# Kernel optimization log

Measured on AMD Instinct MI355X. Metric: run time of the kernel, lower is better.

Reference implementation:

```python
import jax, jax.numpy as jnp
import numpy as np

N_NODES = 100000
N_EDGES = 3200000
D_FEAT = 64
H_SIZE = 32
N_CLASSES = 10


def setup_inputs() -> dict:
    key = jax.random.key(0)
    ks = jax.random.split(key, 9)
    x = jax.random.normal(ks[0], (N_NODES, D_FEAT), dtype=jnp.float32)
    edge_index = jax.random.randint(ks[1], (2, N_EDGES), 0, N_NODES, dtype=jnp.int64)
    y = jax.random.randint(ks[2], (N_NODES,), 0, N_CLASSES, dtype=jnp.int64)
    s1 = 1.0 / np.sqrt(D_FEAT)
    s2 = 1.0 / np.sqrt(H_SIZE)
    W1_rel = jax.random.uniform(ks[3], (H_SIZE, D_FEAT), jnp.float32, -s1, s1)
    b1_rel = jax.random.uniform(ks[4], (H_SIZE,), jnp.float32, -s1, s1)
    W1_root = jax.random.uniform(ks[5], (H_SIZE, D_FEAT), jnp.float32, -s1, s1)
    W2_rel = jax.random.uniform(ks[6], (N_CLASSES, H_SIZE), jnp.float32, -s2, s2)
    b2_rel = jax.random.uniform(ks[7], (N_CLASSES,), jnp.float32, -s2, s2)
    W2_root = jax.random.uniform(ks[8], (N_CLASSES, H_SIZE), jnp.float32, -s2, s2)
    return {"x": x, "edge_index": edge_index, "y": y,
            "W1_rel": W1_rel, "b1_rel": b1_rel, "W1_root": W1_root,
            "W2_rel": W2_rel, "b2_rel": b2_rel, "W2_root": W2_root}


def _graph_conv(x, src, dst, W_rel, b_rel, W_root):
    # PyG GraphConv (aggr='add'): out_i = W_root x_i + b + W_rel * sum_{j: (j->i)} x_j
    agg = jax.ops.segment_sum(x[src], dst, num_segments=N_NODES)  # [N, d_in]
    return agg @ W_rel.T + b_rel + x @ W_root.T


def reference(x, edge_index, y, W1_rel, b1_rel, W1_root, W2_rel, b2_rel, W2_root):
    src, dst = edge_index[0], edge_index[1]
    h = jax.nn.relu(_graph_conv(x, src, dst, W1_rel, b1_rel, W1_root))  # [N, 32]
    logits = _graph_conv(h, src, dst, W2_rel, b2_rel, W2_root)          # [N, 10]
    logp = jax.nn.log_softmax(logits, axis=-1)
    loss = -jnp.mean(jnp.take_along_axis(logp, y[:, None], axis=-1)[:, 0])
    return loss
```

## Files before the change

kernel.cpp:

```cpp
#include <hip/hip_runtime.h>
#include <hip/hip_bf16.h>
#include <hip/hip_fp8.h>

#define D_FEAT 64
#define H_SIZE 32
#define N_CLASSES 10
#define NPB 256
#define MAXB 512
#define NCHUNK 256
#define BT 1024
#define NT 256
#define CSR_CAP 12032

using short8 = __attribute__((ext_vector_type(8))) short;
using f32x4v = __attribute__((ext_vector_type(4))) float;

__device__ inline short f2bf(float f) {
    __hip_bfloat16 h = __float2bfloat16(f);
    return *reinterpret_cast<short*>(&h);
}

#define F8(u, s) ({ __hip_fp8_e4m3 _f; _f.__x = (unsigned char)(((u) >> (s)) & 0xff); (float)_f; })

#define ACC16(p) do { \
    a[0]  += F8((p).x, 0);  a[1]  += F8((p).x, 8);  a[2]  += F8((p).x, 16); a[3]  += F8((p).x, 24); \
    a[4]  += F8((p).y, 0);  a[5]  += F8((p).y, 8);  a[6]  += F8((p).y, 16); a[7]  += F8((p).y, 24); \
    a[8]  += F8((p).z, 0);  a[9]  += F8((p).z, 8);  a[10] += F8((p).z, 16); a[11] += F8((p).z, 24); \
    a[12] += F8((p).w, 0);  a[13] += F8((p).w, 8);  a[14] += F8((p).w, 16); a[15] += F8((p).w, 24); } while (0)

#define ACC8(p) do { \
    a[0] += __uint_as_float((p).x << 16); a[1] += __uint_as_float((p).x & 0xFFFF0000u); \
    a[2] += __uint_as_float((p).y << 16); a[3] += __uint_as_float((p).y & 0xFFFF0000u); \
    a[4] += __uint_as_float((p).z << 16); a[5] += __uint_as_float((p).z & 0xFFFF0000u); \
    a[6] += __uint_as_float((p).w << 16); a[7] += __uint_as_float((p).w & 0xFFFF0000u); } while (0)


__global__ __launch_bounds__(NT) void dense1_mfma(
    const float* __restrict__ x, const float* __restrict__ W1_rel,
    const float* __restrict__ b1, const float* __restrict__ W1_root,
    unsigned* __restrict__ xr8, float* __restrict__ xroot, int n_nodes) {
    __shared__ unsigned short sW[64 * 72];
    __shared__ float sOut[64 * 65];
    __shared__ float sb[H_SIZE];
    int tid = threadIdx.x;
    for (int i = tid; i < 64 * 64; i += NT) {
        int n = i >> 6, k = i & 63;
        float w = (n < 32) ? W1_rel[n * 64 + k] : W1_root[(n - 32) * 64 + k];
        sW[n * 72 + k] = (unsigned short)f2bf(w);
    }
    if (tid < H_SIZE) sb[tid] = b1[tid];
    __syncthreads();

    int lane = tid & 63, wave = tid >> 6;
    int r16 = lane & 15, h = lane >> 4;

    short8 bf[4][2];
#pragma unroll
    for (int t = 0; t < 4; ++t)
#pragma unroll
        for (int s = 0; s < 2; ++s) {
            const unsigned short* p = &sW[(t * 16 + r16) * 72 + s * 32 + h * 8];
            bf[t][s] = *reinterpret_cast<const short8*>(p);
        }

    int nbase = blockIdx.x * 64 + wave * 16;
    int row = nbase + r16;
    int rowc = min(row, n_nodes - 1);

    short8 af[2];
#pragma unroll
    for (int s = 0; s < 2; ++s) {
        const float* px = x + (size_t)rowc * D_FEAT + s * 32 + h * 8;
        float4 lo = *reinterpret_cast<const float4*>(px);
        float4 hi = *reinterpret_cast<const float4*>(px + 4);
        short8 a;
        a[0] = f2bf(lo.x); a[1] = f2bf(lo.y); a[2] = f2bf(lo.z); a[3] = f2bf(lo.w);
        a[4] = f2bf(hi.x); a[5] = f2bf(hi.y); a[6] = f2bf(hi.z); a[7] = f2bf(hi.w);
        af[s] = a;
    }

    f32x4v acc[4] = {{0.f,0.f,0.f,0.f},{0.f,0.f,0.f,0.f},
                     {0.f,0.f,0.f,0.f},{0.f,0.f,0.f,0.f}};
#pragma unroll
    for (int t = 0; t < 4; ++t) {
        acc[t] = __builtin_amdgcn_mfma_f32_16x16x32_bf16(af[0], bf[t][0], acc[t], 0, 0, 0);
        acc[t] = __builtin_amdgcn_mfma_f32_16x16x32_bf16(af[1], bf[t][1], acc[t], 0, 0, 0);
    }
#pragma unroll
    for (int t = 0; t < 4; ++t)
#pragma unroll
        for (int r = 0; r < 4; ++r)
            sOut[(wave * 16 + h * 4 + r) * 65 + t * 16 + r16] = acc[t][r];
    __syncthreads();

    int nl = lane;
    int g = blockIdx.x * 64 + nl;
    if (g < n_nodes) {
        if (wave < 2) {
            unsigned w4[4];
#pragma unroll
            for (int q = 0; q < 4; ++q) {
                unsigned wd = 0;
#pragma unroll
                for (int b = 0; b < 4; ++b) {
                    float v = sOut[nl * 65 + wave * 16 + q * 4 + b];
                    __hip_fp8_e4m3 f8(v);
                    wd |= ((unsigned)f8.__x) << (8 * b);
                }
                w4[q] = wd;
            }
            *reinterpret_cast<uint4*>(&xr8[(size_t)g * 8 + wave * 4]) =
                make_uint4(w4[0], w4[1], w4[2], w4[3]);
        } else {
            int co = (wave - 2) * 16;
#pragma unroll
            for (int q = 0; q < 4; ++q) {
                float4 v;
                v.x = sOut[nl * 65 + 32 + co + q * 4 + 0] + sb[co + q * 4 + 0];
                v.y = sOut[nl * 65 + 32 + co + q * 4 + 1] + sb[co + q * 4 + 1];
                v.z = sOut[nl * 65 + 32 + co + q * 4 + 2] + sb[co + q * 4 + 2];
                v.w = sOut[nl * 65 + 32 + co + q * 4 + 3] + sb[co + q * 4 + 3];
                *reinterpret_cast<float4*>(&xroot[(size_t)g * 32 + co + q * 4]) = v;
            }
        }
    }
}


__global__ __launch_bounds__(BT) void bucket_count(
    const int* __restrict__ dst, int* __restrict__ counts,
    int* __restrict__ totals, int n_edges, int nbuckets, int ept) {
    __shared__ int hist[MAXB];
    for (int i = threadIdx.x; i < nbuckets; i += BT) hist[i] = 0;
    __syncthreads();
    int beg = blockIdx.x * ept;
    int end = min(beg + ept, n_edges);
    for (int e = beg + threadIdx.x; e < end; e += BT)
        atomicAdd(&hist[dst[e] >> 8], 1);
    __syncthreads();
    for (int b = threadIdx.x; b < nbuckets; b += BT) {
        int h = hist[b];
        counts[b * NCHUNK + blockIdx.x] = h;
        if (h) atomicAdd(&totals[b], h);
    }
}

__global__ __launch_bounds__(MAXB) void scan_small(
    const int* __restrict__ totals, int* __restrict__ bbase, int nbuckets) {
    __shared__ int lds[MAXB];
    int tid = threadIdx.x;
    int v = (tid < nbuckets) ? totals[tid] : 0;
    lds[tid] = v;
    __syncthreads();
    for (int off = 1; off < MAXB; off <<= 1) {
        int t = (tid >= off) ? lds[tid - off] : 0;
        __syncthreads();
        lds[tid] += t;
        __syncthreads();
    }
    if (tid < nbuckets) bbase[tid] = lds[tid] - v;
}

__global__ __launch_bounds__(NPB) void scan_within(
    int* __restrict__ counts, const int* __restrict__ bbase) {
    __shared__ int lds[NPB];
    int b = blockIdx.x, tid = threadIdx.x;
    int v = counts[b * NCHUNK + tid];
    lds[tid] = v;
    __syncthreads();
    for (int off = 1; off < NPB; off <<= 1) {
        int t = (tid >= off) ? lds[tid - off] : 0;
        __syncthreads();
        lds[tid] += t;
        __syncthreads();
    }
    counts[b * NCHUNK + tid] = bbase[b] + lds[tid] - v;
}

__global__ __launch_bounds__(BT) void bucket_scatter(
    const int* __restrict__ src, const int* __restrict__ dst,
    const int* __restrict__ base, unsigned* __restrict__ packed,
    int n_edges, int nbuckets, int ept) {
    __shared__ int cur[MAXB];
    for (int b = threadIdx.x; b < nbuckets; b += BT)
        cur[b] = base[b * NCHUNK + blockIdx.x];
    __syncthreads();
    int beg = blockIdx.x * ept;
    int end = min(beg + ept, n_edges);
    for (int e = beg + threadIdx.x; e < end; e += BT) {
        int s = src[e], d = dst[e];
        int slot = atomicAdd(&cur[d >> 8], 1);
        packed[slot] = (unsigned)s | ((unsigned)(d & 255) << 24);
    }
}


__global__ __launch_bounds__(NPB) void csr_build(
    const unsigned* __restrict__ packed, const int* __restrict__ base,
    int* __restrict__ rowptr, int* __restrict__ csr,
    int n_nodes, int nbuckets, int n_edges) {
    __shared__ int cnt[NPB];
    __shared__ int cur[NPB];
    __shared__ unsigned cache[CSR_CAP];
    int b = blockIdx.x, tid = threadIdx.x;
    int pBeg = base[b * NCHUNK];
    int pEnd = (b + 1 < nbuckets) ? base[(b + 1) * NCHUNK] : n_edges;
    int sz = pEnd - pBeg;
    int m = min(sz, CSR_CAP);
    cnt[tid] = 0;
    for (int i = tid; i < m; i += NPB) cache[i] = packed[pBeg + i];
    __syncthreads();
    for (int i = tid; i < sz; i += NPB) {
        unsigned p = (i < m) ? cache[i] : packed[pBeg + i];
        atomicAdd(&cnt[p >> 24], 1);
    }
    __syncthreads();
    int v = cnt[tid];
    cur[tid] = v;
    __syncthreads();
    for (int off = 1; off < NPB; off <<= 1) {
        int t = (tid >= off) ? cur[tid - off] : 0;
        __syncthreads();
        cur[tid] += t;
        __syncthreads();
    }
    int gbase = pBeg + cur[tid] - v;
    int n = (b << 8) + tid;
    if (n < n_nodes) rowptr[n] = gbase;
    if (b == nbuckets - 1 && tid == 0) rowptr[n_nodes] = n_edges;
    cur[tid] = gbase;
    __syncthreads();
    for (int i = tid; i < sz; i += NPB) {
        unsigned p = (i < m) ? cache[i] : packed[pBeg + i];
        int slot = atomicAdd(&cur[p >> 24], 1);
        csr[slot] = (int)(p & 0xFFFFFF);
    }
}


__global__ __launch_bounds__(NT) void gather1_kernel(
    const uint4* __restrict__ xr8v,
    const float* __restrict__ xroot,
    const int* __restrict__ rowptr, const int* __restrict__ csr,
    const float* __restrict__ W2_rel, const float* __restrict__ b2,
    const float* __restrict__ W2_root,
    __hip_bfloat16* __restrict__ h2, float* __restrict__ hroot, int n_nodes) {
    __shared__ float sWrelT[H_SIZE * 17];
    __shared__ float sWrootT[H_SIZE * 17];
    __shared__ float sb[16];
    __shared__ float sh[128][33];
    int tid = threadIdx.x;
    for (int i = tid; i < H_SIZE * 17; i += NT) { sWrelT[i] = 0.f; sWrootT[i] = 0.f; }
    __syncthreads();
    for (int i = tid; i < N_CLASSES * H_SIZE; i += NT) {
        int c = i >> 5, j = i & 31;
        sWrelT[j * 17 + c] = W2_rel[i];
        sWrootT[j * 17 + c] = W2_root[i];
    }
    if (tid < 16) sb[tid] = (tid < N_CLASSES) ? b2[tid] : 0.f;

    int t = blockIdx.x * NT + tid;
    int n = t >> 1, c1 = t & 1;
    float a[16] = {0.f,0.f,0.f,0.f,0.f,0.f,0.f,0.f,
                   0.f,0.f,0.f,0.f,0.f,0.f,0.f,0.f};
    if (n < n_nodes) {
        int beg = rowptr[n], end = rowptr[n + 1];
        int i = beg;
        for (; i + 8 <= end; i += 8) {
            int e0 = csr[i + c1];
            int e1 = csr[i + 2 + c1];
            int e2 = csr[i + 4 + c1];
            int e3 = csr[i + 6 + c1];
            uint4 p0 = xr8v[(size_t)__shfl(e0, 0, 2) * 2 + c1];
            uint4 p1 = xr8v[(size_t)__shfl(e0, 1, 2) * 2 + c1];
            uint4 p2 = xr8v[(size_t)__shfl(e1, 0, 2) * 2 + c1];
            uint4 p3 = xr8v[(size_t)__shfl(e1, 1, 2) * 2 + c1];
            uint4 p4 = xr8v[(size_t)__shfl(e2, 0, 2) * 2 + c1];
            uint4 p5 = xr8v[(size_t)__shfl(e2, 1, 2) * 2 + c1];
            uint4 p6 = xr8v[(size_t)__shfl(e3, 0, 2) * 2 + c1];
            uint4 p7 = xr8v[(size_t)__shfl(e3, 1, 2) * 2 + c1];
            ACC16(p0); ACC16(p1); ACC16(p2); ACC16(p3);
            ACC16(p4); ACC16(p5); ACC16(p6); ACC16(p7);
        }
        if (i + 4 <= end) {
            int e0 = csr[i + c1];
            int e1 = csr[i + 2 + c1];
            uint4 p0 = xr8v[(size_t)__shfl(e0, 0, 2) * 2 + c1];
            uint4 p1 = xr8v[(size_t)__shfl(e0, 1, 2) * 2 + c1];
            uint4 p2 = xr8v[(size_t)__shfl(e1, 0, 2) * 2 + c1];
            uint4 p3 = xr8v[(size_t)__shfl(e1, 1, 2) * 2 + c1];
            ACC16(p0); ACC16(p1); ACC16(p2); ACC16(p3);
            i += 4;
        }
        if (i + 2 <= end) {
            int e0 = csr[i + c1];
            uint4 p0 = xr8v[(size_t)__shfl(e0, 0, 2) * 2 + c1];
            uint4 p1 = xr8v[(size_t)__shfl(e0, 1, 2) * 2 + c1];
            ACC16(p0); ACC16(p1);
            i += 2;
        }
        if (i < end) {
            int e = csr[i];
            uint4 p = xr8v[(size_t)e * 2 + c1];
            ACC16(p);
        }
        const float4* xr4 = reinterpret_cast<const float4*>(
            xroot + (size_t)n * 32 + c1 * 16);
#pragma unroll
        for (int q = 0; q < 4; ++q) {
            float4 v = xr4[q];
            a[q * 4 + 0] = fmaxf(a[q * 4 + 0] + v.x, 0.f);
            a[q * 4 + 1] = fmaxf(a[q * 4 + 1] + v.y, 0.f);
            a[q * 4 + 2] = fmaxf(a[q * 4 + 2] + v.z, 0.f);
            a[q * 4 + 3] = fmaxf(a[q * 4 + 3] + v.w, 0.f);
        }
    }
    int nl = tid >> 1;
#pragma unroll
    for (int j = 0; j < 16; ++j) sh[nl][c1 * 16 + j] = a[j];
    __syncthreads();

#pragma unroll
    for (int pass = 0; pass < 8; ++pass) {
        int idx = pass * NT + tid;
        int nl2 = idx >> 4, c = idx & 15;
        int n2 = blockIdx.x * 128 + nl2;
        if (n2 < n_nodes) {
            float ar = 0.f, ao = 0.f;
#pragma unroll
            for (int j = 0; j < H_SIZE; ++j) {
                float hv = sh[nl2][j];
                ar += hv * sWrelT[j * 17 + c];
                ao += hv * sWrootT[j * 17 + c];
            }
            h2[(size_t)n2 * 16 + c] = __float2bfloat16(ar);
            hroot[(size_t)n2 * 16 + c] = ao + sb[c];
        }
    }
}


__global__ __launch_bounds__(NT) void gather2_loss_kernel(
    const uint4* __restrict__ h2v,
    const float* __restrict__ hroot,
    const int* __restrict__ rowptr, const int* __restrict__ csr,
    const int* __restrict__ y, float* __restrict__ loss,
    int n_nodes, float invN) {
    int t = blockIdx.x * NT + threadIdx.x;
    int n = t >> 1, c1 = t & 1;
    int lane = threadIdx.x & 63;
    bool active = (n < n_nodes);

    float a[8] = {0.f,0.f,0.f,0.f,0.f,0.f,0.f,0.f};
    int yv = 0;
    if (active) {
        int beg = rowptr[n], end = rowptr[n + 1];
        int i = beg;
        for (; i + 8 <= end; i += 8) {
            int e0 = csr[i + c1];
            int e1 = csr[i + 2 + c1];
            int e2 = csr[i + 4 + c1];
            int e3 = csr[i + 6 + c1];
            uint4 p0 = h2v[(size_t)__shfl(e0, 0, 2) * 2 + c1];
            uint4 p1 = h2v[(size_t)__shfl(e0, 1, 2) * 2 + c1];
            uint4 p2 = h2v[(size_t)__shfl(e1, 0, 2) * 2 + c1];
            uint4 p3 = h2v[(size_t)__shfl(e1, 1, 2) * 2 + c1];
            uint4 p4 = h2v[(size_t)__shfl(e2, 0, 2) * 2 + c1];
            uint4 p5 = h2v[(size_t)__shfl(e2, 1, 2) * 2 + c1];
            uint4 p6 = h2v[(size_t)__shfl(e3, 0, 2) * 2 + c1];
            uint4 p7 = h2v[(size_t)__shfl(e3, 1, 2) * 2 + c1];
            ACC8(p0); ACC8(p1); ACC8(p2); ACC8(p3);
            ACC8(p4); ACC8(p5); ACC8(p6); ACC8(p7);
        }
        if (i + 4 <= end) {
            int e0 = csr[i + c1];
            int e1 = csr[i + 2 + c1];
            uint4 p0 = h2v[(size_t)__shfl(e0, 0, 2) * 2 + c1];
            uint4 p1 = h2v[(size_t)__shfl(e0, 1, 2) * 2 + c1];
            uint4 p2 = h2v[(size_t)__shfl(e1, 0, 2) * 2 + c1];
            uint4 p3 = h2v[(size_t)__shfl(e1, 1, 2) * 2 + c1];
            ACC8(p0); ACC8(p1); ACC8(p2); ACC8(p3);
            i += 4;
        }
        if (i + 2 <= end) {
            int e0 = csr[i + c1];
            uint4 p0 = h2v[(size_t)__shfl(e0, 0, 2) * 2 + c1];
            uint4 p1 = h2v[(size_t)__shfl(e0, 1, 2) * 2 + c1];
            ACC8(p0); ACC8(p1);
            i += 2;
        }
        if (i < end) {
            int e = csr[i];
            uint4 p = h2v[(size_t)e * 2 + c1];
            ACC8(p);
        }
        const float4* hr4 = reinterpret_cast<const float4*>(
            hroot + (size_t)n * 16 + c1 * 8);
        float4 h0 = hr4[0], h1 = hr4[1];
        a[0] += h0.x; a[1] += h0.y; a[2] += h0.z; a[3] += h0.w;
        a[4] += h1.x; a[5] += h1.y; a[6] += h1.z; a[7] += h1.w;
        yv = y[n];
    }
    bool full = active && (c1 == 0);
    float m = -INFINITY;
#pragma unroll
    for (int j = 0; j < 8; ++j) {
        bool v = (j < 2) ? active : full;
        m = fmaxf(m, v ? a[j] : -INFINITY);
    }
    m = fmaxf(m, __shfl_xor(m, 1, 64));
    float es = 0.f;
#pragma unroll
    for (int j = 0; j < 8; ++j) {
        bool v = (j < 2) ? active : full;
        es += v ? expf(a[j] - m) : 0.f;
    }
    es += __shfl_xor(es, 1, 64);
    int yl = yv & 7;
    float lyc = 0.f;
#pragma unroll
    for (int j = 0; j < 8; ++j) lyc = (j == yl) ? a[j] : lyc;
    float ly = __shfl(lyc, (lane & ~1) + (yv >> 3), 64);
    float contrib = (active && c1 == 0) ? (m + logf(es) - ly) * invN : 0.f;

#pragma unroll
    for (int o = 32; o > 0; o >>= 1) contrib += __shfl_down(contrib, o, 64);
    __shared__ float part[NT / 64];
    if (lane == 0) part[threadIdx.x >> 6] = contrib;
    __syncthreads();
    if (threadIdx.x == 0) {
        float v = 0.f;
#pragma unroll
        for (int w = 0; w < NT / 64; ++w) v += part[w];
        atomicAdd(loss, v);
    }
}


extern "C" void kernel_launch(void* const* d_in, const int* in_sizes, int n_in,
                              void* d_out, int out_size, void* d_ws, size_t ws_size,
                              hipStream_t stream) {
    const float* x       = (const float*)d_in[0];
    const int*   ei      = (const int*)d_in[1];
    const int*   y       = (const int*)d_in[2];
    const float* W1_rel  = (const float*)d_in[3];
    const float* b1_rel  = (const float*)d_in[4];
    const float* W1_root = (const float*)d_in[5];
    const float* W2_rel  = (const float*)d_in[6];
    const float* b2_rel  = (const float*)d_in[7];
    const float* W2_root = (const float*)d_in[8];
    float* loss = (float*)d_out;

    const int n_nodes = in_sizes[0] / D_FEAT;
    const int n_edges = in_sizes[1] / 2;
    const int* src = ei;
    const int* dst = ei + n_edges;

    const int nbuckets = (n_nodes + NPB - 1) / NPB;
    const int M = nbuckets * NCHUNK;
    const int ept = (n_edges + NCHUNK - 1) / NCHUNK;

    size_t off = 0;
    auto alloc = [&](size_t bytes) {
        void* p = (char*)d_ws + off;
        off = (off + bytes + 255) & ~(size_t)255;
        return p;
    };
    int*            counts = (int*)alloc((size_t)(M + 1) * 4);
    int*            totals = (int*)alloc((size_t)MAXB * 4);
    int*            bbase  = (int*)alloc((size_t)MAXB * 4);
    unsigned*       packed = (unsigned*)alloc((size_t)n_edges * 4);
    int*            rowptr = (int*)alloc((size_t)(n_nodes + 1) * 4);
    int*            csr    = (int*)alloc((size_t)n_edges * 4);
    unsigned*       xr8    = (unsigned*)alloc((size_t)n_nodes * 32);
    float*          xroot  = (float*)alloc((size_t)n_nodes * H_SIZE * 4);
    __hip_bfloat16* h2     = (__hip_bfloat16*)alloc((size_t)n_nodes * 16 * 2);
    float*          hroot  = (float*)alloc((size_t)n_nodes * 16 * 4);

    dense1_mfma<<<(n_nodes + 63) / 64, NT, 0, stream>>>(
        x, W1_rel, b1_rel, W1_root, xr8, xroot, n_nodes);

    hipMemsetAsync(totals, 0, (size_t)MAXB * 4, stream);
    bucket_count<<<NCHUNK, BT, 0, stream>>>(dst, counts, totals,
                                            n_edges, nbuckets, ept);
    scan_small<<<1, MAXB, 0, stream>>>(totals, bbase, nbuckets);
    scan_within<<<nbuckets, NPB, 0, stream>>>(counts, bbase);
    bucket_scatter<<<NCHUNK, BT, 0, stream>>>(src, dst, counts, packed,
                                              n_edges, nbuckets, ept);
    csr_build<<<nbuckets, NPB, 0, stream>>>(packed, counts, rowptr, csr,
                                            n_nodes, nbuckets, n_edges);

    gather1_kernel<<<(n_nodes + 127) / 128, NT, 0, stream>>>(
        (const uint4*)xr8, xroot, rowptr, csr,
        W2_rel, b2_rel, W2_root, h2, hroot, n_nodes);

    hipMemsetAsync(loss, 0, sizeof(float), stream);
    gather2_loss_kernel<<<(n_nodes + 127) / 128, NT, 0, stream>>>(
        (const uint4*)h2, hroot, rowptr, csr, y, loss,
        n_nodes, 1.f / (float)n_nodes);
}
```

Measured before the change: 158.7 us.

## Store layer-2 message features as FP8 and gather whole rows per thread

gather1 now quantises the 16-wide per-node relation projection to FP8 e4m3 and packs four values per word, giving 16-byte rows instead of 32-byte bf16 rows. gather2 changes from two lanes sharing each neighbour row to each lane of a pair loading full 16-byte rows for alternate edges, then combining the pair with xor shuffles. The log-softmax now runs in a single lane over all 10 classes. The aim is to halve the random-gather traffic in the second aggregation, at the cost of FP8 rounding error in the logits and so in the loss.

After: 155.2 us. -2.3%, faster.

```diff
diff --git a/kernel.cpp b/kernel.cpp
--- a/kernel.cpp
+++ b/kernel.cpp
@@ -28,11 +28,10 @@
     a[8]  += F8((p).z, 0);  a[9]  += F8((p).z, 8);  a[10] += F8((p).z, 16); a[11] += F8((p).z, 24); \
     a[12] += F8((p).w, 0);  a[13] += F8((p).w, 8);  a[14] += F8((p).w, 16); a[15] += F8((p).w, 24); } while (0)
 
-#define ACC8(p) do { \
-    a[0] += __uint_as_float((p).x << 16); a[1] += __uint_as_float((p).x & 0xFFFF0000u); \
-    a[2] += __uint_as_float((p).y << 16); a[3] += __uint_as_float((p).y & 0xFFFF0000u); \
-    a[4] += __uint_as_float((p).z << 16); a[5] += __uint_as_float((p).z & 0xFFFF0000u); \
-    a[6] += __uint_as_float((p).w << 16); a[7] += __uint_as_float((p).w & 0xFFFF0000u); } while (0)
+#define ACC10(p) do { \
+    a[0] += F8((p).x, 0);  a[1] += F8((p).x, 8);  a[2] += F8((p).x, 16); a[3] += F8((p).x, 24); \
+    a[4] += F8((p).y, 0);  a[5] += F8((p).y, 8);  a[6] += F8((p).y, 16); a[7] += F8((p).y, 24); \
+    a[8] += F8((p).z, 0);  a[9] += F8((p).z, 8); } while (0)
 
 
 __global__ __launch_bounds__(NT) void dense1_mfma(
@@ -244,7 +243,7 @@
     const int* __restrict__ rowptr, const int* __restrict__ csr,
     const float* __restrict__ W2_rel, const float* __restrict__ b2,
     const float* __restrict__ W2_root,
-    __hip_bfloat16* __restrict__ h2, float* __restrict__ hroot, int n_nodes) {
+    unsigned* __restrict__ h2b, float* __restrict__ hroot, int n_nodes) {
     __shared__ float sWrelT[H_SIZE * 17];
     __shared__ float sWrootT[H_SIZE * 17];
     __shared__ float sb[16];
@@ -325,15 +324,24 @@
         int idx = pass * NT + tid;
         int nl2 = idx >> 4, c = idx & 15;
         int n2 = blockIdx.x * 128 + nl2;
-        if (n2 < n_nodes) {
-            float ar = 0.f, ao = 0.f;
-#pragma unroll
-            for (int j = 0; j < H_SIZE; ++j) {
-                float hv = sh[nl2][j];
-                ar += hv * sWrelT[j * 17 + c];
-                ao += hv * sWrootT[j * 17 + c];
+        bool valid = (n2 < n_nodes);
+        float ar = 0.f, ao = 0.f;
+#pragma unroll
+        for (int j = 0; j < H_SIZE; ++j) {
+            float hv = sh[nl2][j];
+            ar += hv * sWrelT[j * 17 + c];
+            ao += hv * sWrootT[j * 17 + c];
+        }
+        float r1 = __shfl_down(ar, 1, 64);
+        float r2 = __shfl_down(ar, 2, 64);
+        float r3 = __shfl_down(ar, 3, 64);
+        if (valid) {
+            if ((c & 3) == 0) {
+                __hip_fp8_e4m3 f0(ar), f1(r1), f2(r2), f3(r3);
+                unsigned wd = (unsigned)f0.__x | ((unsigned)f1.__x << 8) |
+                              ((unsigned)f2.__x << 16) | ((unsigned)f3.__x << 24);
+                h2b[(size_t)n2 * 4 + (c >> 2)] = wd;
             }
-            h2[(size_t)n2 * 16 + c] = __float2bfloat16(ar);
             hroot[(size_t)n2 * 16 + c] = ao + sb[c];
         }
     }
@@ -341,7 +349,7 @@
 
 
 __global__ __launch_bounds__(NT) void gather2_loss_kernel(
-    const uint4* __restrict__ h2v,
+    const uint4* __restrict__ h2q,
     const float* __restrict__ hroot,
     const int* __restrict__ rowptr, const int* __restrict__ csr,
     const int* __restrict__ y, float* __restrict__ loss,
@@ -351,8 +359,7 @@
     int lane = threadIdx.x & 63;
     bool active = (n < n_nodes);
 
-    float a[8] = {0.f,0.f,0.f,0.f,0.f,0.f,0.f,0.f};
-    int yv = 0;
+    float a[10] = {0.f,0.f,0.f,0.f,0.f,0.f,0.f,0.f,0.f,0.f};
     if (active) {
         int beg = rowptr[n], end = rowptr[n + 1];
         int i = beg;
@@ -361,67 +368,46 @@
             int e1 = csr[i + 2 + c1];
             int e2 = csr[i + 4 + c1];
             int e3 = csr[i + 6 + c1];
-            uint4 p0 = h2v[(size_t)__shfl(e0, 0, 2) * 2 + c1];
-            uint4 p1 = h2v[(size_t)__shfl(e0, 1, 2) * 2 + c1];
-            uint4 p2 = h2v[(size_t)__shfl(e1, 0, 2) * 2 + c1];
-            uint4 p3 = h2v[(size_t)__shfl(e1, 1, 2) * 2 + c1];
-            uint4 p4 = h2v[(size_t)__shfl(e2, 0, 2) * 2 + c1];
-            uint4 p5 = h2v[(size_t)__shfl(e2, 1, 2) * 2 + c1];
-            uint4 p6 = h2v[(size_t)__shfl(e3, 0, 2) * 2 + c1];
-            uint4 p7 = h2v[(size_t)__shfl(e3, 1, 2) * 2 + c1];
-            ACC8(p0); ACC8(p1); ACC8(p2); ACC8(p3);
-            ACC8(p4); ACC8(p5); ACC8(p6); ACC8(p7);
-        }
-        if (i + 4 <= end) {
+            uint4 p0 = h2q[e0];
+            uint4 p1 = h2q[e1];
+            uint4 p2 = h2q[e2];
+            uint4 p3 = h2q[e3];
+            ACC10(p0); ACC10(p1); ACC10(p2); ACC10(p3);
+        }
+        for (; i + 2 <= end; i += 2) {
             int e0 = csr[i + c1];
-            int e1 = csr[i + 2 + c1];
-            uint4 p0 = h2v[(size_t)__shfl(e0, 0, 2) * 2 + c1];
-            uint4 p1 = h2v[(size_t)__shfl(e0, 1, 2) * 2 + c1];
-            uint4 p2 = h2v[(size_t)__shfl(e1, 0, 2) * 2 + c1];
-            uint4 p3 = h2v[(size_t)__shfl(e1, 1, 2) * 2 + c1];
-            ACC8(p0); ACC8(p1); ACC8(p2); ACC8(p3);
-            i += 4;
-        }
-        if (i + 2 <= end) {
-            int e0 = csr[i + c1];
-            uint4 p0 = h2v[(size_t)__shfl(e0, 0, 2) * 2 + c1];
-            uint4 p1 = h2v[(size_t)__shfl(e0, 1, 2) * 2 + c1];
-            ACC8(p0); ACC8(p1);
-            i += 2;
-        }
-        if (i < end) {
-            int e = csr[i];
-            uint4 p = h2v[(size_t)e * 2 + c1];
-            ACC8(p);
-        }
-        const float4* hr4 = reinterpret_cast<const float4*>(
-            hroot + (size_t)n * 16 + c1 * 8);
-        float4 h0 = hr4[0], h1 = hr4[1];
+            uint4 p0 = h2q[e0];
+            ACC10(p0);
+        }
+        if (i < end && c1 == 0) {
+            uint4 p = h2q[csr[i]];
+            ACC10(p);
+        }
+    }
+#pragma unroll
+    for (int j = 0; j < N_CLASSES; ++j) a[j] += __shfl_xor(a[j], 1, 64);
+
+    float contrib = 0.f;
+    if (active && c1 == 0) {
+        const float* hr = hroot + (size_t)n * 16;
+        float4 h0 = *reinterpret_cast<const float4*>(hr);
+        float4 h1 = *reinterpret_cast<const float4*>(hr + 4);
+        float2 hx = *reinterpret_cast<const float2*>(hr + 8);
         a[0] += h0.x; a[1] += h0.y; a[2] += h0.z; a[3] += h0.w;
         a[4] += h1.x; a[5] += h1.y; a[6] += h1.z; a[7] += h1.w;
-        yv = y[n];
-    }
-    bool full = active && (c1 == 0);
-    float m = -INFINITY;
-#pragma unroll
-    for (int j = 0; j < 8; ++j) {
-        bool v = (j < 2) ? active : full;
-        m = fmaxf(m, v ? a[j] : -INFINITY);
-    }
-    m = fmaxf(m, __shfl_xor(m, 1, 64));
-    float es = 0.f;
-#pragma unroll
-    for (int j = 0; j < 8; ++j) {
-        bool v = (j < 2) ? active : full;
-        es += v ? expf(a[j] - m) : 0.f;
-    }
-    es += __shfl_xor(es, 1, 64);
-    int yl = yv & 7;
-    float lyc = 0.f;
-#pragma unroll
-    for (int j = 0; j < 8; ++j) lyc = (j == yl) ? a[j] : lyc;
-    float ly = __shfl(lyc, (lane & ~1) + (yv >> 3), 64);
-    float contrib = (active && c1 == 0) ? (m + logf(es) - ly) * invN : 0.f;
+        a[8] += hx.x; a[9] += hx.y;
+        int yv = y[n];
+        float m = a[0];
+#pragma unroll
+        for (int j = 1; j < N_CLASSES; ++j) m = fmaxf(m, a[j]);
+        float es = 0.f;
+#pragma unroll
+        for (int j = 0; j < N_CLASSES; ++j) es += expf(a[j] - m);
+        float ly = a[0];
+#pragma unroll
+        for (int j = 1; j < N_CLASSES; ++j) ly = (j == yv) ? a[j] : ly;
+        contrib = (m + logf(es) - ly) * invN;
+    }
 
 #pragma unroll
     for (int o = 32; o > 0; o >>= 1) contrib += __shfl_down(contrib, o, 64);
@@ -466,16 +452,16 @@
         off = (off + bytes + 255) & ~(size_t)255;
         return p;
     };
-    int*            counts = (int*)alloc((size_t)(M + 1) * 4);
-    int*            totals = (int*)alloc((size_t)MAXB * 4);
-    int*            bbase  = (int*)alloc((size_t)MAXB * 4);
-    unsigned*       packed = (unsigned*)alloc((size_t)n_edges * 4);
-    int*            rowptr = (int*)alloc((size_t)(n_nodes + 1) * 4);
-    int*            csr    = (int*)alloc((size_t)n_edges * 4);
-    unsigned*       xr8    = (unsigned*)alloc((size_t)n_nodes * 32);
-    float*          xroot  = (float*)alloc((size_t)n_nodes * H_SIZE * 4);
-    __hip_bfloat16* h2     = (__hip_bfloat16*)alloc((size_t)n_nodes * 16 * 2);
-    float*          hroot  = (float*)alloc((size_t)n_nodes * 16 * 4);
+    int*      counts = (int*)alloc((size_t)(M + 1) * 4);
+    int*      totals = (int*)alloc((size_t)MAXB * 4);
+    int*      bbase  = (int*)alloc((size_t)MAXB * 4);
+    unsigned* packed = (unsigned*)alloc((size_t)n_edges * 4);
+    int*      rowptr = (int*)alloc((size_t)(n_nodes + 1) * 4);
+    int*      csr    = (int*)alloc((size_t)n_edges * 4);
+    unsigned* xr8    = (unsigned*)alloc((size_t)n_nodes * 32);
+    float*    xroot  = (float*)alloc((size_t)n_nodes * H_SIZE * 4);
+    unsigned* h2b    = (unsigned*)alloc((size_t)n_nodes * 16);
+    float*    hroot  = (float*)alloc((size_t)n_nodes * 16 * 4);
 
     dense1_mfma<<<(n_nodes + 63) / 64, NT, 0, stream>>>(
         x, W1_rel, b1_rel, W1_root, xr8, xroot, n_nodes);
@@ -492,10 +478,10 @@
 
     gather1_kernel<<<(n_nodes + 127) / 128, NT, 0, stream>>>(
         (const uint4*)xr8, xroot, rowptr, csr,
-        W2_rel, b2_rel, W2_root, h2, hroot, n_nodes);
+        W2_rel, b2_rel, W2_root, h2b, hroot, n_nodes);
 
     hipMemsetAsync(loss, 0, sizeof(float), stream);
     gather2_loss_kernel<<<(n_nodes + 127) / 128, NT, 0, stream>>>(
-        (const uint4*)h2, hroot, rowptr, csr, y, loss,
+        (const uint4*)h2b, hroot, rowptr, csr, y, loss,
         n_nodes, 1.f / (float)n_nodes);
 }
```
